# Kernel optimization log

Hardware: AMD Instinct MI355X
Metric: run time of the kernel (lower is better)

Reference implementation:

```python
import jax, jax.numpy as jnp
import numpy as np

LAPLACIAN = jnp.array([[-1., -1., -1.], [-1., 8., -1.], [-1., -1., -1.]], dtype=jnp.float32)


def setup_inputs() -> dict:
    key = jax.random.key(0)
    k1, k2 = jax.random.split(key)
    pred = jax.random.normal(k1, (8, 19, 512, 512), dtype=jnp.float32)
    target = jax.random.randint(k2, (8, 512, 512), 0, 19, dtype=jnp.int32)
    return {"pred": pred, "target": target}


def _boundary(x):
    # x: [B, C, H, W] -> abs(clamp(laplacian(x))) per (batch, class) plane
    B, C, H, W = x.shape
    xr = x.reshape(B * C, 1, H, W)
    kern = LAPLACIAN[None, None, :, :]  # [O=1, I=1, 3, 3]
    y = jax.lax.conv_general_dilated(xr, kern, window_strides=(1, 1), padding="SAME")
    return jnp.clip(jnp.abs(y), 0.0, 1.0).reshape(B, C, H, W)


def reference(pred, target):
    # softmax over class dim
    p = jax.nn.softmax(pred, axis=1)
    B, C, H, W = p.shape
    # one-hot target masks: (target[i] == c).float()
    onehot = (target[:, None, :, :] == jnp.arange(C, dtype=target.dtype)[None, :, None, None]).astype(p.dtype)
    pb = _boundary(p)
    tb = _boundary(onehot)
    # sum over (b,c) of per-plane MSE, / (B*C)  == global mean of squared diff
    return jnp.mean((pb - tb) ** 2)
```

## Files before the change

kernel.cpp:

```cpp
#include <hip/hip_runtime.h>

#define NB 8
#define NC 19
#define NH 512
#define NW 512
#define HWP (NH * NW)

#define TW 32
#define TH 16
#define HB_W 40
#define HB_H 18
#define PLANE (HB_W * HB_H)
#define NQ_W 9
#define NQUAD (HB_H * NQ_W)
#define NPAIR 10
#define NTHREADS 256
#define NBLOCKS 4096

typedef _Float16 h2 __attribute__((ext_vector_type(2)));

static __device__ __forceinline__ unsigned int h2_to_u(h2 v) {
    return __builtin_bit_cast(unsigned int, v);
}
static __device__ __forceinline__ h2 u_to_h2(unsigned int u) {
    return __builtin_bit_cast(h2, u);
}

#if __has_builtin(__builtin_amdgcn_cvt_pkrtz)
static __device__ __forceinline__ h2 cvt_pk2(float a, float b) {
    return __builtin_bit_cast(h2, __builtin_amdgcn_cvt_pkrtz(a, b));
}
#else
static __device__ __forceinline__ h2 cvt_pk2(float a, float b) {
    h2 r; r[0] = (_Float16)a; r[1] = (_Float16)b; return r;
}
#endif

#if __has_builtin(__builtin_amdgcn_fdot2)
static __device__ __forceinline__ float fdot2f(h2 a, h2 b, float c) {
    return __builtin_amdgcn_fdot2(a, b, c, false);
}
#else
static __device__ __forceinline__ float fdot2f(h2 a, h2 b, float c) {
    return c + (float)a[0] * (float)b[0] + (float)a[1] * (float)b[1];
}
#endif

__global__ __launch_bounds__(NTHREADS, 5) void bl_main(
    const float* __restrict__ pred, const int* __restrict__ target,
    float* __restrict__ partial)
{
    __shared__ unsigned int e_lds[NPAIR][PLANE];
    __shared__ int t_lds[PLANE];

    const int tid = threadIdx.x;
    const int n = blockIdx.x;
    const int tI = ((n & 7) << 9) + (n >> 3);
    const int bz = tI >> 9;
    const int rem = tI & 511;
    const int by = rem >> 4;
    const int bx = rem & 15;

    const int h0 = by * TH - 1;
    const int gxq = bx * TW - 2;
    const float* predb = pred + (size_t)bz * NC * HWP;
    const int* tgtb = target + (size_t)bz * HWP;

    if (tid < NQUAD) {
        const int r = tid / NQ_W;
        const int q = tid - r * NQ_W;
        const int gh = h0 + r;
        const int gq = gxq + (q << 2);
        const int ghc = min(max(gh, 0), NH - 1);
        const int gqc = min(max(gq, 0), NW - 4);
        const bool rowok = (gh >= 0) && (gh < NH);
        const float* src = predb + (size_t)ghc * NW + gqc;

        const int4 tv = *reinterpret_cast<const int4*>(
            tgtb + (size_t)ghc * NW + gqc);

        float s0 = 0.f, s1 = 0.f, s2 = 0.f, s3 = 0.f;
        unsigned int pkv[NPAIR][4];

        #pragma unroll
        for (int j = 0; j < NPAIR; ++j) {
            const float4 a = *reinterpret_cast<const float4*>(
                src + (size_t)(2 * j) * HWP);
            const float ea0 = __expf(a.x), ea1 = __expf(a.y);
            const float ea2 = __expf(a.z), ea3 = __expf(a.w);
            float eb0 = 0.f, eb1 = 0.f, eb2 = 0.f, eb3 = 0.f;
            if (j < NPAIR - 1) {
                const float4 b = *reinterpret_cast<const float4*>(
                    src + (size_t)(2 * j + 1) * HWP);
                eb0 = __expf(b.x); eb1 = __expf(b.y);
                eb2 = __expf(b.z); eb3 = __expf(b.w);
            }
            s0 += ea0 + eb0; s1 += ea1 + eb1;
            s2 += ea2 + eb2; s3 += ea3 + eb3;
            pkv[j][0] = h2_to_u(cvt_pk2(ea0, eb0));
            pkv[j][1] = h2_to_u(cvt_pk2(ea1, eb1));
            pkv[j][2] = h2_to_u(cvt_pk2(ea2, eb2));
            pkv[j][3] = h2_to_u(cvt_pk2(ea3, eb3));
        }

        #define NORM_PX(E, SE, OK)                                          \
        {                                                                   \
            const float invf = (OK) ? __builtin_amdgcn_rcpf(SE) : 0.f;      \
            const _Float16 ih = (_Float16)invf;                             \
            h2 ih2v; ih2v[0] = ih; ih2v[1] = ih;                            \
            _Pragma("unroll")                                               \
            for (int j = 0; j < NPAIR; ++j)                                 \
                pkv[j][E] = h2_to_u(u_to_h2(pkv[j][E]) * ih2v);             \
        }
        const bool ok0 = rowok && (gq + 0 >= 0) && (gq + 0 < NW);
        const bool ok1 = rowok && (gq + 1 >= 0) && (gq + 1 < NW);
        const bool ok2 = rowok && (gq + 2 >= 0) && (gq + 2 < NW);
        const bool ok3 = rowok && (gq + 3 >= 0) && (gq + 3 < NW);
        NORM_PX(0, s0, ok0) NORM_PX(1, s1, ok1)
        NORM_PX(2, s2, ok2) NORM_PX(3, s3, ok3)
        #undef NORM_PX

        const int lb = r * HB_W + 2 + (q << 2);
        #pragma unroll
        for (int j = 0; j < NPAIR; ++j) {
            uint2* d = reinterpret_cast<uint2*>(&e_lds[j][lb]);
            d[0] = make_uint2(pkv[j][0], pkv[j][1]);
            d[1] = make_uint2(pkv[j][2], pkv[j][3]);
        }

        int2* td = reinterpret_cast<int2*>(&t_lds[lb]);
        td[0] = make_int2(ok0 ? tv.x : 31, ok1 ? tv.y : 31);
        td[1] = make_int2(ok2 ? tv.z : 31, ok3 ? tv.w : 31);
    }
    __syncthreads();

    float acc = 0.f;
    if (tid >= 128) {
        const int t = tid - 128;
        const int u = t & 15;
        const int s = t >> 4;
        const int r0 = 2 * s;
        const int cw = 2 * u + 2;

        int w[4][4];
        #pragma unroll
        for (int r = 0; r < 4; ++r) {
            const int base = (r0 + r) * HB_W + cw;
            const int2 mdl = *reinterpret_cast<const int2*>(&t_lds[base + 2]);
            w[r][0] = t_lds[base + 1];
            w[r][1] = mdl.x;
            w[r][2] = mdl.y;
            w[r][3] = t_lds[base + 4];
        }

        unsigned int rm[2][4];
        #pragma unroll
        for (int r = 0; r < 4; ++r) {
            const unsigned b1 = 1u << w[r][0];
            const unsigned b2 = 1u << w[r][1];
            const unsigned b3 = 1u << w[r][2];
            const unsigned b4 = 1u << w[r][3];
            const unsigned mm = b2 | b3;
            rm[0][r] = mm | b1;
            rm[1][r] = mm | b4;
        }
        unsigned int mpx[2][2];
        #pragma unroll
        for (int jc = 0; jc < 2; ++jc) {
            const unsigned mid = rm[jc][1] | rm[jc][2];
            #pragma unroll
            for (int k = 0; k < 2; ++k) {
                unsigned m = mid | rm[jc][k ? 3 : 0];
                m = (__popc(m) == 1) ? 0u : (m & 0x7FFFFu);
                mpx[jc][k] = m;
                acc += (float)__popc(m);
            }
        }

        h2 one2;  one2[0] = (_Float16)1.f;  one2[1] = (_Float16)1.f;
        h2 nine2; nine2[0] = (_Float16)9.f; nine2[1] = (_Float16)9.f;

        #pragma unroll
        for (int j = 0; j < NPAIR; ++j) {
            const unsigned int* plane = &e_lds[j][0];
            h2 rs[2][4];
            h2 ctr[2][2];
            #pragma unroll
            for (int r = 0; r < 4; ++r) {
                const int base = (r0 + r) * HB_W + cw;
                const uint2 pm = *reinterpret_cast<const uint2*>(&plane[base + 2]);
                const h2 v1 = u_to_h2(plane[base + 1]);
                const h2 v2 = u_to_h2(pm.x);
                const h2 v3 = u_to_h2(pm.y);
                const h2 v4 = u_to_h2(plane[base + 4]);
                const h2 tm = v2 + v3;
                rs[0][r] = v1 + tm;
                rs[1][r] = tm + v4;
                if (r == 1) { ctr[0][0] = v2; ctr[1][0] = v3; }
                if (r == 2) { ctr[0][1] = v2; ctr[1][1] = v3; }
            }
            #pragma unroll
            for (int jc = 0; jc < 2; ++jc) {
                const h2 midv = rs[jc][1] + rs[jc][2];
                #pragma unroll
                for (int k = 0; k < 2; ++k) {
                    const h2 S = midv + rs[jc][k ? 3 : 0];
                    const h2 lap = ctr[jc][k] * nine2 - S;
                    const h2 ab = u_to_h2(h2_to_u(lap) & 0x7FFF7FFFu);
                    h2 mn;
                    mn[0] = ab[0] < one2[0] ? ab[0] : one2[0];
                    mn[1] = ab[1] < one2[1] ? ab[1] : one2[1];
                    acc = fdot2f(mn, mn, acc);
                    const unsigned bits = (mpx[jc][k] >> (2 * j)) & 3u;
                    const unsigned nt = (bits & 1u ? 0x0000C000u : 0u) |
                                        (bits & 2u ? 0xC0000000u : 0u);
                    acc = fdot2f(mn, u_to_h2(nt), acc);
                }
            }
        }
    }

    #pragma unroll
    for (int off = 32; off > 0; off >>= 1)
        acc += __shfl_down(acc, off, 64);

    __shared__ float wsum[NTHREADS / 64];
    if ((tid & 63) == 0) wsum[tid >> 6] = acc;
    __syncthreads();
    if (tid == 0) {
        float s = 0.f;
        #pragma unroll
        for (int i = 0; i < NTHREADS / 64; ++i) s += wsum[i];
        partial[n] = s;
    }
}

__global__ __launch_bounds__(1024) void bl_reduce(
    const float4* __restrict__ partial, float* __restrict__ out)
{
    const float4 v = partial[threadIdx.x];
    float s = v.x + v.y + v.z + v.w;
    #pragma unroll
    for (int off = 32; off > 0; off >>= 1)
        s += __shfl_down(s, off, 64);
    __shared__ float wsum[16];
    if ((threadIdx.x & 63) == 0) wsum[threadIdx.x >> 6] = s;
    __syncthreads();
    if (threadIdx.x == 0) {
        float t = 0.f;
        #pragma unroll
        for (int i = 0; i < 16; ++i) t += wsum[i];
        out[0] = t * (1.0f / ((float)NB * NC * NH * NW));
    }
}

extern "C" void kernel_launch(void* const* d_in, const int* in_sizes, int n_in,
                              void* d_out, int out_size, void* d_ws, size_t ws_size,
                              hipStream_t stream) {
    const float* pred = (const float*)d_in[0];
    const int* target = (const int*)d_in[1];
    float* partial = (float*)d_ws;

    bl_main<<<dim3(NBLOCKS), NTHREADS, 0, stream>>>(pred, target, partial);
    bl_reduce<<<1, 1024, 0, stream>>>((const float4*)partial, (float*)d_out);
}
```

Baseline: 38.01 us.

## Halve tile height to double blocks and fold reduction into atomics

Tile height drops from 16 to 8 rows, which doubles the block count to 8192, shrinks per-block LDS and raises the occupancy hint to 7. Only one wave now does the compute phase instead of two. The separate reduction kernel is removed: the output is zeroed with a memset and each block atomically adds its scaled partial sum. This cuts per-block LDS and one launch, but adds more halo rows relative to useful rows, thousands of atomics on a single address, and a nondeterministic summation order.

```diff
diff --git a/kernel.cpp b/kernel.cpp
--- a/kernel.cpp
+++ b/kernel.cpp
@@ -7,15 +7,15 @@
 #define HWP (NH * NW)
 
 #define TW 32
-#define TH 16
+#define TH 8
 #define HB_W 40
-#define HB_H 18
+#define HB_H 10
 #define PLANE (HB_W * HB_H)
 #define NQ_W 9
 #define NQUAD (HB_H * NQ_W)
 #define NPAIR 10
 #define NTHREADS 256
-#define NBLOCKS 4096
+#define NBLOCKS 8192
 
 typedef _Float16 h2 __attribute__((ext_vector_type(2)));
 
@@ -46,18 +46,18 @@
 }
 #endif
 
-__global__ __launch_bounds__(NTHREADS, 5) void bl_main(
+__global__ __launch_bounds__(NTHREADS, 7) void bl_main(
     const float* __restrict__ pred, const int* __restrict__ target,
-    float* __restrict__ partial)
+    float* __restrict__ out)
 {
     __shared__ unsigned int e_lds[NPAIR][PLANE];
     __shared__ int t_lds[PLANE];
 
     const int tid = threadIdx.x;
     const int n = blockIdx.x;
-    const int tI = ((n & 7) << 9) + (n >> 3);
-    const int bz = tI >> 9;
-    const int rem = tI & 511;
+    const int tI = ((n & 7) << 10) + (n >> 3);
+    const int bz = tI >> 10;
+    const int rem = tI & 1023;
     const int by = rem >> 4;
     const int bx = rem & 15;
 
@@ -135,8 +135,8 @@
     __syncthreads();
 
     float acc = 0.f;
-    if (tid >= 128) {
-        const int t = tid - 128;
+    if (tid >= 192) {
+        const int t = tid - 192;
         const int u = t & 15;
         const int s = t >> 4;
         const int r0 = 2 * s;
@@ -228,29 +228,8 @@
     if ((tid & 63) == 0) wsum[tid >> 6] = acc;
     __syncthreads();
     if (tid == 0) {
-        float s = 0.f;
-        #pragma unroll
-        for (int i = 0; i < NTHREADS / 64; ++i) s += wsum[i];
-        partial[n] = s;
-    }
-}
-
-__global__ __launch_bounds__(1024) void bl_reduce(
-    const float4* __restrict__ partial, float* __restrict__ out)
-{
-    const float4 v = partial[threadIdx.x];
-    float s = v.x + v.y + v.z + v.w;
-    #pragma unroll
-    for (int off = 32; off > 0; off >>= 1)
-        s += __shfl_down(s, off, 64);
-    __shared__ float wsum[16];
-    if ((threadIdx.x & 63) == 0) wsum[threadIdx.x >> 6] = s;
-    __syncthreads();
-    if (threadIdx.x == 0) {
-        float t = 0.f;
-        #pragma unroll
-        for (int i = 0; i < 16; ++i) t += wsum[i];
-        out[0] = t * (1.0f / ((float)NB * NC * NH * NW));
+        const float s = wsum[0] + wsum[1] + wsum[2] + wsum[3];
+        atomicAdd(out, s * (1.0f / ((float)NB * NC * NH * NW)));
     }
 }
 
@@ -259,8 +238,8 @@
                               hipStream_t stream) {
     const float* pred = (const float*)d_in[0];
     const int* target = (const int*)d_in[1];
-    float* partial = (float*)d_ws;
-
-    bl_main<<<dim3(NBLOCKS), NTHREADS, 0, stream>>>(pred, target, partial);
-    bl_reduce<<<1, 1024, 0, stream>>>((const float4*)partial, (float*)d_out);
-}
+
+    hipMemsetAsync(d_out, 0, sizeof(float), stream);
+    bl_main<<<dim3(NBLOCKS), NTHREADS, 0, stream>>>(
+        pred, target, (float*)d_out);
+}
```

Result: slower. 133.1 us (+250.2%).
